# Kernel optimization log

Hardware: AMD Instinct MI355X
Metric: run time of the kernel (lower is better)

## Reference

```python
import jax, jax.numpy as jnp
import numpy as np

N = 50000        # nodes
E = 800000       # edges (avg degree 16)
F_IN = 256       # input features
H1 = 8           # heads, layer 1
F1 = 256 // H1   # per-head out features, layer 1 (n_hid//heads)
N_HID = H1 * F1  # 256
N_CLASS = 47     # classes (layer 2: 1 head)


def setup_inputs() -> dict:
    key = jax.random.key(0)
    ks = jax.random.split(key, 12)
    s = 0.05
    x = jax.random.normal(ks[0], (N, F_IN), dtype=jnp.float32)
    edge_src = jax.random.randint(ks[1], (E,), 0, N, dtype=jnp.int32)
    edge_dst = jax.random.randint(ks[2], (E,), 0, N, dtype=jnp.int32)
    W1 = jax.random.normal(ks[3], (F_IN, F1), dtype=jnp.float32) * s
    Wl1 = jax.random.normal(ks[4], (F1, H1), dtype=jnp.float32) * s
    Wr1 = jax.random.normal(ks[5], (F1, H1), dtype=jnp.float32) * s
    b1 = jax.random.normal(ks[6], (F1,), dtype=jnp.float32) * s
    W2 = jax.random.normal(ks[7], (N_HID, N_CLASS), dtype=jnp.float32) * s
    Wl2 = jax.random.normal(ks[8], (N_CLASS, 1), dtype=jnp.float32) * s
    Wr2 = jax.random.normal(ks[9], (N_CLASS, 1), dtype=jnp.float32) * s
    b2 = jax.random.normal(ks[10], (N_CLASS,), dtype=jnp.float32) * s
    return {"x": x, "edge_src": edge_src, "edge_dst": edge_dst,
            "W1": W1, "Wl1": Wl1, "Wr1": Wr1, "b1": b1,
            "W2": W2, "Wl2": Wl2, "Wr2": Wr2, "b2": b2}


def gat_conv(x, src, dst, W, Wl, Wr, b):
    # x: [N,Fin], W: [Fin,F], Wl/Wr: [F,H], b: [F]
    n_nodes = x.shape[0]
    h = x @ W                                  # [N,F]
    el = h @ Wl                                # [N,H]
    er = h @ Wr                                # [N,H]
    # per-edge attention: exp(leaky_relu(el_i + er_j)) for edge (i=src, j=dst)
    e = jnp.exp(jax.nn.leaky_relu(el[src] + er[dst], negative_slope=0.2))  # [E,H]
    # segment softmax denominator over outgoing edges of each row i
    # (matches F.normalize(p=1, dim=-1) with eps=1e-12 on nonneg entries)
    denom = jnp.maximum(jax.ops.segment_sum(e, src, num_segments=n_nodes), 1e-12)  # [N,H]
    # weighted aggregation: out[i,h,:] = sum_{e: src=i} a_e[h] * repr[dst_e]
    msg = e[:, :, None] * h[dst][:, None, :]   # [E,H,F]
    agg = jax.ops.segment_sum(msg, src, num_segments=n_nodes)  # [N,H,F]
    out = agg / denom[:, :, None] + b          # bias broadcasts over heads
    if out.shape[1] > 1:
        return out.reshape(n_nodes, -1)        # flatten heads: [N,H*F]
    return out[:, 0, :]                        # [N,F]


def reference(x, edge_src, edge_dst, W1, Wl1, Wr1, b1, W2, Wl2, Wr2, b2):
    r = gat_conv(x, edge_src, edge_dst, W1, Wl1, Wr1, b1)   # [N, 256]
    r = jax.nn.elu(r)                                        # activation (dropout: eval no-op)
    r = gat_conv(r, edge_src, edge_dst, W2, Wl2, Wr2, b2)    # [N, 47]
    return jax.nn.log_softmax(r, axis=1)
```

## Files before the change

### kernel.cpp

```cpp
#include <hip/hip_runtime.h>

#define N_NODES 50000
#define N_EDGES 800000
#define F_IN 256
#define H1 8
#define N_HID 256
#define N_CLASS 47
#define MAXDEG 48
#define NW16 (N_NODES/16)
#define G1BLK ((NW16 + 3) / 4)

#define BSH 7
#define RNG 128
#define NBUCK 391
#define CAP 2560
#define HBLK 256
#define CHUNK (N_EDGES/HBLK)
#define PREB 82

typedef __attribute__((ext_vector_type(8))) __bf16 bf16x8;
typedef __attribute__((ext_vector_type(4))) float f32x4;

__device__ __forceinline__ float bf2f(unsigned short u){
    union { unsigned int i; float f; } c; c.i = ((unsigned int)u) << 16; return c.f;
}
__device__ __forceinline__ unsigned short f2b(float f){
    union { float f; unsigned int i; } c; c.f = f;
    unsigned int u = c.i;
    unsigned int r = u + 0x7FFFu + ((u >> 16) & 1u);
    return (unsigned short)(r >> 16);
}

__global__ void k_pre(const float* __restrict__ W1,
                      const float* __restrict__ W2,
                      const float* __restrict__ Wl1,
                      const float* __restrict__ Wr1,
                      unsigned short* __restrict__ bp1,
                      unsigned short* __restrict__ bp2,
                      unsigned short* __restrict__ bp3,
                      int* __restrict__ cursor){
    int tid = blockIdx.x * blockDim.x + threadIdx.x;
    if (tid < NBUCK) cursor[tid] = tid * CAP;
    if (tid < 8*2*64*8) {
        int j = tid & 7, lane = (tid >> 3) & 63, tile = (tid >> 9) & 1, kc = tid >> 10;
        int k = kc*32 + (lane >> 4)*8 + j;
        int n = tile*16 + (lane & 15);
        bp1[tid] = f2b(W1[k*32 + n]);
    }
    int t2 = tid - 8192;
    if (t2 >= 0 && t2 < 8*3*64*8) {
        int j = t2 & 7, lane = (t2 >> 3) & 63;
        int tile = (t2 >> 9) % 3, kc = t2 / 1536;
        int k = kc*32 + (lane >> 4)*8 + j;
        int n = tile*16 + (lane & 15);
        bp2[t2] = (n < N_CLASS) ? f2b(W2[k*N_CLASS + n]) : (unsigned short)0;
    }
    int t3 = tid - 20480;
    if (t3 >= 0 && t3 < 512) {
        int j = t3 & 7, lane = t3 >> 3;
        int n = lane & 15, k = (lane >> 4)*8 + j;
        bp3[t3] = (n < 8) ? f2b(Wl1[k*8 + n]) : f2b(Wr1[k*8 + (n - 8)]);
    }
}

__global__ __launch_bounds__(256)
void k_fg(const float* __restrict__ x,
          const unsigned short* __restrict__ bp1,
          const unsigned short* __restrict__ bp3,
          unsigned short* __restrict__ h1b,
          float* __restrict__ el1, float* __restrict__ er1,
          const int* __restrict__ src, const int* __restrict__ dst,
          int* __restrict__ cursor, unsigned int* __restrict__ sorted){
    __shared__ __align__(16) unsigned short lds_h[4][16][40];
    __shared__ int lhist[NBUCK], lbase[NBUCK], lcur[NBUCK];
    if (blockIdx.x >= G1BLK){
        int b = blockIdx.x - G1BLK;
        for (int k = threadIdx.x; k < NBUCK; k += 256){ lhist[k] = 0; lcur[k] = 0; }
        __syncthreads();
        int e0 = b * CHUNK;
        for (int i = threadIdx.x; i < CHUNK; i += 256){
            int s = src[e0 + i];
            s = ((unsigned)s < N_NODES) ? s : 0;
            atomicAdd(&lhist[s >> BSH], 1);
        }
        __syncthreads();
        for (int k = threadIdx.x; k < NBUCK; k += 256){
            int c = lhist[k];
            lbase[k] = c ? atomicAdd(&cursor[k], c) : 0;
        }
        __syncthreads();
        for (int i = threadIdx.x; i < CHUNK; i += 256){
            int s = src[e0 + i];
            s = ((unsigned)s < N_NODES) ? s : 0;
            unsigned int d = (unsigned int)dst[e0 + i] & 0xffffu;
            int k = s >> BSH;
            int p = atomicAdd(&lcur[k], 1);
            int idx = lbase[k] + p;
            if (idx < (k + 1) * CAP)
                sorted[idx] = ((unsigned int)s << 16) | d;
        }
        return;
    }
    int w = threadIdx.x >> 6;
    int wid = (blockIdx.x * blockDim.x + threadIdx.x) >> 6;
    int lane = threadIdx.x & 63;
    if (wid >= NW16) return;
    int m0 = wid * 16;
    int mrow = m0 + (lane & 15);
    int q = lane >> 4;
    f32x4 z = {0.f,0.f,0.f,0.f};
    f32x4 acc0 = z, acc1 = z;
    const float* xrow = x + (size_t)mrow * F_IN + q * 8;
    #pragma unroll
    for (int kc = 0; kc < 8; kc++){
        const f32x4* xp = (const f32x4*)(xrow + kc*32);
        f32x4 u0 = xp[0], u1 = xp[1];
        union { bf16x8 v; unsigned short s[8]; } ua;
        ua.s[0]=f2b(u0[0]); ua.s[1]=f2b(u0[1]); ua.s[2]=f2b(u0[2]); ua.s[3]=f2b(u0[3]);
        ua.s[4]=f2b(u1[0]); ua.s[5]=f2b(u1[1]); ua.s[6]=f2b(u1[2]); ua.s[7]=f2b(u1[3]);
        bf16x8 b0 = *reinterpret_cast<const bf16x8*>(bp1 + kc*1024 + lane*8);
        bf16x8 b1 = *reinterpret_cast<const bf16x8*>(bp1 + kc*1024 + 512 + lane*8);
        acc0 = __builtin_amdgcn_mfma_f32_16x16x32_bf16(ua.v, b0, acc0, 0, 0, 0);
        acc1 = __builtin_amdgcn_mfma_f32_16x16x32_bf16(ua.v, b1, acc1, 0, 0, 0);
    }
    int col = lane & 15, rbase = q * 4;
    #pragma unroll
    for (int r = 0; r < 4; r++){
        int row = m0 + rbase + r;
        unsigned short v0 = f2b(acc0[r]), v1 = f2b(acc1[r]);
        h1b[(size_t)row*32 + col]      = v0;
        h1b[(size_t)row*32 + 16 + col] = v1;
        lds_h[w][rbase + r][col]      = v0;
        lds_h[w][rbase + r][16 + col] = v1;
    }
    bf16x8 a2 = *reinterpret_cast<const bf16x8*>(&lds_h[w][lane & 15][q*8]);
    bf16x8 b3 = *reinterpret_cast<const bf16x8*>(bp3 + lane*8);
    f32x4 e = z;
    e = __builtin_amdgcn_mfma_f32_16x16x32_bf16(a2, b3, e, 0, 0, 0);
    #pragma unroll
    for (int r = 0; r < 4; r++){
        int row = m0 + rbase + r;
        if (col < 8) el1[(size_t)row*8 + col]     = e[r];
        else         er1[(size_t)row*8 + col - 8] = e[r];
    }
}

__global__ __launch_bounds__(256)
void k_csr(const unsigned int* __restrict__ sorted,
           const int* __restrict__ cursor,
           unsigned short* __restrict__ csrp, int* __restrict__ cnt){
    __shared__ __align__(16) unsigned short rows[RNG][MAXDEG];
    __shared__ int lcnt[RNG];
    int bkt = blockIdx.x;
    int n0 = bkt << BSH;
    int t = threadIdx.x;
    for (int k = t; k < RNG; k += 256) lcnt[k] = 0;
    __syncthreads();
    int s0 = bkt * CAP;
    int nb = min(cursor[bkt] - s0, CAP);
    for (int i = t; i < nb; i += 256){
        unsigned int e = sorted[s0 + i];
        int ls = (int)(e >> 16) - n0;
        int p = atomicAdd(&lcnt[ls], 1);
        if (p < MAXDEG) rows[ls][p] = (unsigned short)(e & 0xffffu);
    }
    __syncthreads();
    int nn = min(RNG, N_NODES - n0);
    for (int k = t; k < nn; k += 256) cnt[n0 + k] = lcnt[k];
    const uint4* rsrc = (const uint4*)&rows[0][0];
    uint4* rdst = (uint4*)(csrp + (size_t)n0 * MAXDEG);
    int nq = nn * MAXDEG / 8;
    for (int k = t; k < nq; k += 256) rdst[k] = rsrc[k];
}

__global__ __launch_bounds__(256)
void k_agg1g2(const unsigned short* __restrict__ h1b,
              const float* __restrict__ el1, const float* __restrict__ er1,
              const float* __restrict__ b1,
              const float* __restrict__ Wl2, const float* __restrict__ Wr2,
              const int* __restrict__ cnt, const unsigned short* __restrict__ csrp,
              const unsigned short* __restrict__ bp2,
              unsigned short* __restrict__ h2b,
              float* __restrict__ el2, float* __restrict__ er2){
    __shared__ __align__(16) unsigned short lds_r[16][264];
    __shared__ float lds_p[2][3][16];
    int w = threadIdx.x >> 6, lane = threadIdx.x & 63;
    int q = lane >> 4, m = lane & 15;
    int hm = m & 7;
    int base = blockIdx.x * 16;
    int node0 = base + w * 4;
    int4 n4 = *(const int4*)(cnt + node0);
    int n_[4] = { min(n4.x, MAXDEG), min(n4.y, MAXDEG),
                  min(n4.z, MAXDEG), min(n4.w, MAXDEG) };
    float elh[4];
    #pragma unroll
    for (int i = 0; i < 4; i++) elh[i] = el1[(node0 + i)*8 + hm];
    float bv0 = b1[m], bv1 = b1[16 + m];
    #pragma unroll
    for (int i = 0; i < 4; i++){
        int n = n_[i];
        float el_h = elh[i];
        const unsigned short* lst = csrp + (size_t)(node0 + i) * MAXDEG;
        f32x4 acc0 = {0.f,0.f,0.f,0.f}, acc1 = {0.f,0.f,0.f,0.f};
        float dsum = 0.f;
        int nkb = (n + 31) >> 5;
        for (int kb = 0; kb < nkb; kb++){
            int s0 = kb*32 + q*8;
            uint4 idp = *(const uint4*)(lst + s0);
            int idr[8] = { (int)(idp.x & 0xffff), (int)(idp.x >> 16),
                           (int)(idp.y & 0xffff), (int)(idp.y >> 16),
                           (int)(idp.z & 0xffff), (int)(idp.z >> 16),
                           (int)(idp.w & 0xffff), (int)(idp.w >> 16) };
            #pragma unroll
            for (int j = 0; j < 8; j++) idr[j] = (idr[j] < N_NODES) ? idr[j] : 0;
            float wv[8];
            #pragma unroll
            for (int j = 0; j < 8; j++){
                float t = el_h + er1[idr[j]*8 + hm];
                t = (t > 0.f) ? t : 0.2f * t;
                float ev = __expf(fminf(t, 60.f));
                wv[j] = ((s0 + j) < n && m < 8) ? ev : 0.f;
            }
            dsum += ((wv[0]+wv[1])+(wv[2]+wv[3])) + ((wv[4]+wv[5])+(wv[6]+wv[7]));
            union { bf16x8 v; unsigned short s8[8]; } ua;
            #pragma unroll
            for (int j = 0; j < 8; j++) ua.s8[j] = f2b(wv[j]);
            union { bf16x8 v; unsigned short s8[8]; } ub0, ub1;
            #pragma unroll
            for (int j = 0; j < 8; j++){
                const unsigned short* hr = h1b + (size_t)idr[j]*32;
                ub0.s8[j] = hr[m];
                ub1.s8[j] = hr[16 + m];
            }
            acc0 = __builtin_amdgcn_mfma_f32_16x16x32_bf16(ua.v, ub0.v, acc0, 0, 0, 0);
            acc1 = __builtin_amdgcn_mfma_f32_16x16x32_bf16(ua.v, ub1.v, acc1, 0, 0, 0);
        }
        dsum += __shfl_xor(dsum, 16);
        dsum += __shfl_xor(dsum, 32);
        float inv = 1.f / fmaxf(dsum, 1e-12f);
        float ivr[4];
        #pragma unroll
        for (int r = 0; r < 4; r++) ivr[r] = __shfl(inv, 4*q + r);
        if (q < 2){
            #pragma unroll
            for (int r = 0; r < 4; r++){
                int head = 4*q + r;
                float o0 = acc0[r]*ivr[r] + bv0;
                float o1 = acc1[r]*ivr[r] + bv1;
                o0 = (o0 > 0.f) ? o0 : (__expf(o0) - 1.f);
                o1 = (o1 > 0.f) ? o1 : (__expf(o1) - 1.f);
                lds_r[w*4 + i][head*32 + m]      = f2b(o0);
                lds_r[w*4 + i][head*32 + 16 + m] = f2b(o1);
            }
        }
    }
    __syncthreads();
    if (w < 3){
        f32x4 accd = {0.f,0.f,0.f,0.f};
        #pragma unroll
        for (int kc = 0; kc < 8; kc++){
            bf16x8 a = *reinterpret_cast<const bf16x8*>(&lds_r[m][kc*32 + q*8]);
            bf16x8 b = *reinterpret_cast<const bf16x8*>(bp2 + kc*1536 + w*512 + lane*8);
            accd = __builtin_amdgcn_mfma_f32_16x16x32_bf16(a, b, accd, 0, 0, 0);
        }
        int col = m, rbase = q * 4;
        int cls = w*16 + col;
        float wl2v = (cls < N_CLASS) ? Wl2[cls] : 0.f;
        float wr2v = (cls < N_CLASS) ? Wr2[cls] : 0.f;
        float pe[4], pr[4];
        #pragma unroll
        for (int r = 0; r < 4; r++){
            int grow = base + rbase + r;
            h2b[(size_t)grow*48 + w*16 + col] = f2b(accd[r]);
            pe[r] = accd[r] * wl2v;
            pr[r] = accd[r] * wr2v;
        }
        #pragma unroll
        for (int msk = 1; msk <= 8; msk <<= 1){
            #pragma unroll
            for (int r = 0; r < 4; r++){
                pe[r] += __shfl_xor(pe[r], msk);
                pr[r] += __shfl_xor(pr[r], msk);
            }
        }
        if (col == 0){
            #pragma unroll
            for (int r = 0; r < 4; r++){
                lds_p[0][w][rbase + r] = pe[r];
                lds_p[1][w][rbase + r] = pr[r];
            }
        }
    }
    __syncthreads();
    if (w == 3 && lane < 16){
        float ev = lds_p[0][0][lane] + lds_p[0][1][lane] + lds_p[0][2][lane];
        float rv = lds_p[1][0][lane] + lds_p[1][1][lane] + lds_p[1][2][lane];
        el2[base + lane] = ev;
        er2[base + lane] = rv;
    }
}

__global__ __launch_bounds__(256)
void k_agg2(const unsigned short* __restrict__ h2b,
            const float* __restrict__ el2, const float* __restrict__ er2,
            const float* __restrict__ b2,
            const int* __restrict__ cnt, const unsigned short* __restrict__ csrp,
            float* __restrict__ out){
    int wid = (blockIdx.x * blockDim.x + threadIdx.x) >> 6;
    if (wid >= N_NODES) return;
    int lane = threadIdx.x & 63;
    int n = min(cnt[wid], MAXDEG);
    const unsigned short* lst = csrp + (size_t)wid * MAXDEG;
    float el_i = el2[wid];
    int   d_l = 0;
    float w_l = 0.f;
    if (lane < n){
        int dd = (int)lst[lane];
        d_l = (dd < N_NODES) ? dd : 0;
        float t = el_i + er2[d_l];
        t = (t > 0.f) ? t : 0.2f * t;
        w_l = __expf(fminf(t, 60.f));
    }
    float ds = w_l;
    #pragma unroll
    for (int m = 32; m >= 1; m >>= 1) ds += __shfl_xor(ds, m);
    bool valid = lane < N_CLASS;
    int cl = valid ? lane : 0;
    float acc0=0.f, acc1=0.f, acc2=0.f, acc3=0.f;
    for (int e = 0; e < n; e += 8){
        float we0 = __shfl(w_l, e);   int de0 = __shfl(d_l, e);
        float we1 = __shfl(w_l, e+1); int de1 = __shfl(d_l, e+1);
        float we2 = __shfl(w_l, e+2); int de2 = __shfl(d_l, e+2);
        float we3 = __shfl(w_l, e+3); int de3 = __shfl(d_l, e+3);
        float we4 = __shfl(w_l, e+4); int de4 = __shfl(d_l, e+4);
        float we5 = __shfl(w_l, e+5); int de5 = __shfl(d_l, e+5);
        float we6 = __shfl(w_l, e+6); int de6 = __shfl(d_l, e+6);
        float we7 = __shfl(w_l, e+7); int de7 = __shfl(d_l, e+7);
        acc0 += we0 * bf2f(h2b[(size_t)de0*48 + cl]);
        acc1 += we1 * bf2f(h2b[(size_t)de1*48 + cl]);
        acc2 += we2 * bf2f(h2b[(size_t)de2*48 + cl]);
        acc3 += we3 * bf2f(h2b[(size_t)de3*48 + cl]);
        acc0 += we4 * bf2f(h2b[(size_t)de4*48 + cl]);
        acc1 += we5 * bf2f(h2b[(size_t)de5*48 + cl]);
        acc2 += we6 * bf2f(h2b[(size_t)de6*48 + cl]);
        acc3 += we7 * bf2f(h2b[(size_t)de7*48 + cl]);
    }
    float acc = (acc0 + acc1) + (acc2 + acc3);
    float o = acc / fmaxf(ds, 1e-12f) + b2[cl];
    float zm = valid ? o : -1e30f;
    #pragma unroll
    for (int m = 32; m >= 1; m >>= 1) zm = fmaxf(zm, __shfl_xor(zm, m));
    float ex = valid ? __expf(fminf(o - zm, 0.f)) : 0.f;
    #pragma unroll
    for (int m = 32; m >= 1; m >>= 1) ex += __shfl_xor(ex, m);
    float res = o - zm - __logf(ex);
    if (valid) out[(size_t)wid*N_CLASS + lane] = res;
}

extern "C" void kernel_launch(void* const* d_in, const int* in_sizes, int n_in,
                              void* d_out, int out_size, void* d_ws, size_t ws_size,
                              hipStream_t stream){
    const float* x   = (const float*)d_in[0];
    const int*   esrc= (const int*)d_in[1];
    const int*   edst= (const int*)d_in[2];
    const float* W1  = (const float*)d_in[3];
    const float* Wl1 = (const float*)d_in[4];
    const float* Wr1 = (const float*)d_in[5];
    const float* b1  = (const float*)d_in[6];
    const float* W2  = (const float*)d_in[7];
    const float* Wl2 = (const float*)d_in[8];
    const float* Wr2 = (const float*)d_in[9];
    const float* b2  = (const float*)d_in[10];
    float* out = (float*)d_out;

    char* w = (char*)d_ws;
    auto carve = [&](size_t bytes) -> char* {
        char* p = w; w += (bytes + 255) & ~(size_t)255; return p;
    };
    int*            cnt  = (int*)            carve((size_t)N_NODES * 4);
    unsigned short* csrp = (unsigned short*) carve((size_t)N_NODES * MAXDEG * 2);
    unsigned short* h1b  = (unsigned short*) carve((size_t)N_NODES * 32 * 2);
    float*          el1  = (float*)          carve((size_t)N_NODES * 8 * 4);
    float*          er1  = (float*)          carve((size_t)N_NODES * 8 * 4);
    unsigned short* h2b  = (unsigned short*) carve((size_t)N_NODES * 48 * 2);
    float*          el2  = (float*)          carve((size_t)N_NODES * 4);
    float*          er2  = (float*)          carve((size_t)N_NODES * 4);
    unsigned short* bp1  = (unsigned short*) carve(8192 * 2);
    unsigned short* bp2  = (unsigned short*) carve(12288 * 2);
    unsigned short* bp3  = (unsigned short*) carve(512 * 2);
    unsigned int*   sorted = (unsigned int*) carve((size_t)NBUCK * CAP * 4);
    int*            cursor = (int*)          carve((size_t)NBUCK * 4);

    k_pre    <<<PREB, 256, 0, stream>>>(W1, W2, Wl1, Wr1, bp1, bp2, bp3, cursor);
    k_fg     <<<G1BLK + HBLK, 256, 0, stream>>>(x, bp1, bp3, h1b, el1, er1,
                                                esrc, edst, cursor, sorted);
    k_csr    <<<NBUCK, 256, 0, stream>>>(sorted, cursor, csrp, cnt);
    k_agg1g2 <<<NW16, 256, 0, stream>>>(h1b, el1, er1, b1, Wl2, Wr2, cnt, csrp, bp2, h2b, el2, er2);
    k_agg2   <<<(N_NODES + 3) / 4, 256, 0, stream>>>(h2b, el2, er2, b2, cnt, csrp, out);
}
```

Before: 200.8 us.

## Rewrite layer-2 aggregation with MFMA, four nodes per wavefront

Layer-2 aggregation now assigns four nodes per wavefront (16 per block) instead of one node per wave. Each group of 16 lanes handles one node's edge list, and a masked block-diagonal bf16 MFMA 16x16x32 does the weighted sum over neighbours' 47 class features. The aim is to cut per-node shuffle and scalar FMA overhead and raise lane utilisation. The cost is that attention weights are rounded to bf16, most of the MFMA work is wasted on zero-masked entries, and each wave loops to the maximum degree of its four nodes.

```diff
diff --git a/kernel.cpp b/kernel.cpp
--- a/kernel.cpp
+++ b/kernel.cpp
@@ -306,55 +306,80 @@
             const float* __restrict__ b2,
             const int* __restrict__ cnt, const unsigned short* __restrict__ csrp,
             float* __restrict__ out){
-    int wid = (blockIdx.x * blockDim.x + threadIdx.x) >> 6;
-    if (wid >= N_NODES) return;
-    int lane = threadIdx.x & 63;
-    int n = min(cnt[wid], MAXDEG);
-    const unsigned short* lst = csrp + (size_t)wid * MAXDEG;
-    float el_i = el2[wid];
-    int   d_l = 0;
-    float w_l = 0.f;
-    if (lane < n){
-        int dd = (int)lst[lane];
-        d_l = (dd < N_NODES) ? dd : 0;
-        float t = el_i + er2[d_l];
-        t = (t > 0.f) ? t : 0.2f * t;
-        w_l = __expf(fminf(t, 60.f));
-    }
-    float ds = w_l;
-    #pragma unroll
-    for (int m = 32; m >= 1; m >>= 1) ds += __shfl_xor(ds, m);
-    bool valid = lane < N_CLASS;
-    int cl = valid ? lane : 0;
-    float acc0=0.f, acc1=0.f, acc2=0.f, acc3=0.f;
-    for (int e = 0; e < n; e += 8){
-        float we0 = __shfl(w_l, e);   int de0 = __shfl(d_l, e);
-        float we1 = __shfl(w_l, e+1); int de1 = __shfl(d_l, e+1);
-        float we2 = __shfl(w_l, e+2); int de2 = __shfl(d_l, e+2);
-        float we3 = __shfl(w_l, e+3); int de3 = __shfl(d_l, e+3);
-        float we4 = __shfl(w_l, e+4); int de4 = __shfl(d_l, e+4);
-        float we5 = __shfl(w_l, e+5); int de5 = __shfl(d_l, e+5);
-        float we6 = __shfl(w_l, e+6); int de6 = __shfl(d_l, e+6);
-        float we7 = __shfl(w_l, e+7); int de7 = __shfl(d_l, e+7);
-        acc0 += we0 * bf2f(h2b[(size_t)de0*48 + cl]);
-        acc1 += we1 * bf2f(h2b[(size_t)de1*48 + cl]);
-        acc2 += we2 * bf2f(h2b[(size_t)de2*48 + cl]);
-        acc3 += we3 * bf2f(h2b[(size_t)de3*48 + cl]);
-        acc0 += we4 * bf2f(h2b[(size_t)de4*48 + cl]);
-        acc1 += we5 * bf2f(h2b[(size_t)de5*48 + cl]);
-        acc2 += we6 * bf2f(h2b[(size_t)de6*48 + cl]);
-        acc3 += we7 * bf2f(h2b[(size_t)de7*48 + cl]);
-    }
-    float acc = (acc0 + acc1) + (acc2 + acc3);
-    float o = acc / fmaxf(ds, 1e-12f) + b2[cl];
-    float zm = valid ? o : -1e30f;
-    #pragma unroll
-    for (int m = 32; m >= 1; m >>= 1) zm = fmaxf(zm, __shfl_xor(zm, m));
-    float ex = valid ? __expf(fminf(o - zm, 0.f)) : 0.f;
-    #pragma unroll
-    for (int m = 32; m >= 1; m >>= 1) ex += __shfl_xor(ex, m);
-    float res = o - zm - __logf(ex);
-    if (valid) out[(size_t)wid*N_CLASS + lane] = res;
+    int w = threadIdx.x >> 6, lane = threadIdx.x & 63;
+    int q = lane >> 4, m = lane & 15;
+    int node0 = blockIdx.x * 16 + w * 4;
+    int4 n4 = *(const int4*)(cnt + node0);
+    int maxn = min(max(max(n4.x, n4.y), max(n4.z, n4.w)), MAXDEG);
+    int nq = min(cnt[node0 + q], MAXDEG);
+    float el_q = el2[node0 + q];
+    const unsigned short* lst = csrp + (size_t)(node0 + q) * MAXDEG;
+    float bv[3];
+    #pragma unroll
+    for (int t = 0; t < 3; t++){
+        int c = t*16 + m;
+        bv[t] = (c < N_CLASS) ? b2[c] : 0.f;
+    }
+    f32x4 z = {0.f,0.f,0.f,0.f};
+    f32x4 acc0 = z, acc1 = z, acc2 = z;
+    float dsum = 0.f;
+    int rounds = (maxn + 7) >> 3;
+    for (int kb = 0; kb < rounds; kb++){
+        uint4 idp = *(const uint4*)(lst + kb*8);
+        int idr[8] = { (int)(idp.x & 0xffff), (int)(idp.x >> 16),
+                       (int)(idp.y & 0xffff), (int)(idp.y >> 16),
+                       (int)(idp.z & 0xffff), (int)(idp.z >> 16),
+                       (int)(idp.w & 0xffff), (int)(idp.w >> 16) };
+        #pragma unroll
+        for (int j = 0; j < 8; j++) idr[j] = (idr[j] < N_NODES) ? idr[j] : 0;
+        float wv[8];
+        #pragma unroll
+        for (int j = 0; j < 8; j++){
+            float t = el_q + er2[idr[j]];
+            t = (t > 0.f) ? t : 0.2f * t;
+            float ev = __expf(fminf(t, 60.f));
+            wv[j] = ((kb*8 + j) < nq) ? ev : 0.f;
+        }
+        dsum += ((wv[0]+wv[1])+(wv[2]+wv[3])) + ((wv[4]+wv[5])+(wv[6]+wv[7]));
+        union { bf16x8 v; unsigned short s8[8]; } ua;
+        #pragma unroll
+        for (int j = 0; j < 8; j++) ua.s8[j] = (m == q) ? f2b(wv[j]) : (unsigned short)0;
+        union { bf16x8 v; unsigned short s8[8]; } ub0, ub1, ub2;
+        #pragma unroll
+        for (int j = 0; j < 8; j++){
+            const unsigned short* hr = h2b + (size_t)idr[j]*48;
+            ub0.s8[j] = hr[m];
+            ub1.s8[j] = hr[16 + m];
+            ub2.s8[j] = hr[32 + m];
+        }
+        acc0 = __builtin_amdgcn_mfma_f32_16x16x32_bf16(ua.v, ub0.v, acc0, 0, 0, 0);
+        acc1 = __builtin_amdgcn_mfma_f32_16x16x32_bf16(ua.v, ub1.v, acc1, 0, 0, 0);
+        acc2 = __builtin_amdgcn_mfma_f32_16x16x32_bf16(ua.v, ub2.v, acc2, 0, 0, 0);
+    }
+    float inv = 1.f / fmaxf(dsum, 1e-12f);
+    float ivr[4];
+    #pragma unroll
+    for (int r = 0; r < 4; r++) ivr[r] = __shfl(inv, r*16 + m);
+    if (q == 0){
+        #pragma unroll
+        for (int r = 0; r < 4; r++){
+            float o0 = acc0[r]*ivr[r] + bv[0];
+            float o1 = acc1[r]*ivr[r] + bv[1];
+            float o2 = acc2[r]*ivr[r] + bv[2];
+            bool v2 = (32 + m) < N_CLASS;
+            float zm = fmaxf(fmaxf(o0, o1), v2 ? o2 : -1e30f);
+            #pragma unroll
+            for (int msk = 1; msk <= 8; msk <<= 1) zm = fmaxf(zm, __shfl_xor(zm, msk));
+            float ex = __expf(o0 - zm) + __expf(o1 - zm) + (v2 ? __expf(o2 - zm) : 0.f);
+            #pragma unroll
+            for (int msk = 1; msk <= 8; msk <<= 1) ex += __shfl_xor(ex, msk);
+            float lse = zm + __logf(ex);
+            float* op = out + (size_t)(node0 + r) * N_CLASS;
+            op[m]      = o0 - lse;
+            op[16 + m] = o1 - lse;
+            if (v2) op[32 + m] = o2 - lse;
+        }
+    }
 }
 
 extern "C" void kernel_launch(void* const* d_in, const int* in_sizes, int n_in,
@@ -396,5 +421,5 @@
                                                 esrc, edst, cursor, sorted);
     k_csr    <<<NBUCK, 256, 0, stream>>>(sorted, cursor, csrp, cnt);
     k_agg1g2 <<<NW16, 256, 0, stream>>>(h1b, el1, er1, b1, Wl2, Wr2, cnt, csrp, bp2, h2b, el2, er2);
-    k_agg2   <<<(N_NODES + 3) / 4, 256, 0, stream>>>(h2b, el2, er2, b2, cnt, csrp, out);
-}
+    k_agg2   <<<NW16, 256, 0, stream>>>(h2b, el2, er2, b2, cnt, csrp, out);
+}
```

After: 189.6 us. 1.06x faster.
